# Performance work log

Hardware: AMD Instinct MI355X
Metric: run time of the kernel (lower is better)

## Reference

```python
import jax, jax.numpy as jnp
import numpy as np

N = 50000          # nodes
E = 800000         # edges (before self-loops)
IN_CH = 128
HID = 64
HEADS = 4
OUT_CH = 16
NEG_SLOPE = 0.2    # PyG GATConv default leaky_relu slope
EPS = 1e-16        # PyG softmax denominator epsilon


def glorot(key, shape):
    fan_in, fan_out = shape[0], shape[-1]
    lim = np.sqrt(6.0 / (fan_in + fan_out))
    return jax.random.uniform(key, shape, jnp.float32, -lim, lim)


def setup_inputs() -> dict:
    key = jax.random.key(0)
    ks = jax.random.split(key, 12)
    x = jax.random.normal(ks[0], (N, IN_CH), jnp.float32)
    edge_index = jax.random.randint(ks[1], (2, E), 0, N, jnp.int32)
    # layer 1: in -> HID per head, HEADS heads
    W1 = glorot(ks[2], (IN_CH, HEADS * HID))
    a_src1 = glorot(ks[3], (HEADS, HID))
    a_dst1 = glorot(ks[4], (HEADS, HID))
    b1 = jnp.zeros((HEADS * HID,), jnp.float32)
    # layer 2: HEADS*HID -> OUT_CH, 1 head
    W2 = glorot(ks[5], (HEADS * HID, OUT_CH))
    a_src2 = glorot(ks[6], (1, OUT_CH))
    a_dst2 = glorot(ks[7], (1, OUT_CH))
    b2 = jnp.zeros((OUT_CH,), jnp.float32)
    return {"x": x, "edge_index": edge_index,
            "W1": W1, "a_src1": a_src1, "a_dst1": a_dst1, "b1": b1,
            "W2": W2, "a_src2": a_src2, "a_dst2": a_dst2, "b2": b2}


def gat_conv(x, edge_index, W, a_src, a_dst, b, heads, ch):
    """PyG GATConv: linear, edge attention, segment softmax over dst, scatter-agg."""
    n = x.shape[0]
    loops = jnp.arange(n, dtype=edge_index.dtype)
    src = jnp.concatenate([edge_index[0], loops])   # add_self_loops=True
    dst = jnp.concatenate([edge_index[1], loops])
    h = (x @ W).reshape(n, heads, ch)               # [N, H, C]
    s_src = jnp.einsum('nhc,hc->nh', h, a_src)      # [N, H]
    s_dst = jnp.einsum('nhc,hc->nh', h, a_dst)
    e = s_src[src] + s_dst[dst]                     # [E', H]
    e = jnp.where(e > 0, e, NEG_SLOPE * e)          # leaky_relu
    m = jax.ops.segment_max(e, dst, num_segments=n)  # per-dst max
    ex = jnp.exp(e - m[dst])
    denom = jax.ops.segment_sum(ex, dst, num_segments=n)
    alpha = ex / (denom[dst] + EPS)                 # [E', H]
    out = jax.ops.segment_sum(h[src] * alpha[:, :, None], dst, num_segments=n)
    return out.reshape(n, heads * ch) + b


def reference(x, edge_index, W1, a_src1, a_dst1, b1, W2, a_src2, a_dst2, b2):
    h = gat_conv(x, edge_index, W1, a_src1, a_dst1, b1, HEADS, HID)
    h = jax.nn.elu(h)
    return gat_conv(h, edge_index, W2, a_src2, a_dst2, b2, 1, OUT_CH)
```

## Files before the change

### kernel.cpp

```cpp
#include <hip/hip_runtime.h>
#include <cstdint>
#include <cstddef>

#define NN 50000
#define IN_CH 128
#define C1 256
#define HID 64
#define HEADS 4
#define OUT_CH 16
#define NEG_SLOPE 0.2f
#define EPS_SM 1e-16f
#define NEGINF -3.4e38f
#define NBUK ((NN + 255) >> 8)

typedef __attribute__((ext_vector_type(8))) short bf16x8;
typedef __attribute__((ext_vector_type(4))) float f32x4;

__device__ __forceinline__ unsigned short f2b(float f) {
    unsigned int u = __float_as_uint(f);
    u += 0x7fffu + ((u >> 16) & 1u);
    return (unsigned short)(u >> 16);
}
__device__ __forceinline__ float b2f_lo(unsigned int packed) {
    return __uint_as_float(packed << 16);
}
__device__ __forceinline__ float b2f_hi(unsigned int packed) {
    return __uint_as_float(packed & 0xffff0000u);
}

__global__ void cvt_weights(const float* __restrict__ W1, const float* __restrict__ W2,
                            unsigned short* __restrict__ w1t, unsigned short* __restrict__ w2b) {
    int b = blockIdx.x, t = threadIdx.x;
    if (b < 128) {
        w1t[t * 128 + b] = f2b(W1[b * 256 + t]);
    } else {
        int k = (b - 128) * 16 + (t >> 4);
        int c = t & 15;
        w2b[c * 256 + k] = f2b(W2[k * 16 + c]);
    }
}

__global__ __launch_bounds__(256) void gemm1_mfma(const float* __restrict__ X,
                                                  const unsigned short* __restrict__ w1t,
                                                  const float* __restrict__ a_src1,
                                                  const float* __restrict__ a_dst1,
                                                  unsigned short* __restrict__ h1b,
                                                  float* __restrict__ ssrc1,
                                                  float* __restrict__ sdst1, int M) {
    __shared__ unsigned short xb[64 * 128];
    __shared__ unsigned short wt[256 * 128];
    int tid = threadIdx.x;
    int m0 = blockIdx.x * 64;
    {
        const uint4* gp = (const uint4*)w1t;
#pragma unroll
        for (int r = 0; r < 16; ++r) {
            int idx = r * 256 + tid;
            int byte = idx * 16;
            int row = byte >> 8;
            int cb = byte & 255;
            uint4 v = gp[idx];
            *(uint4*)((char*)wt + row * 256 + (cb ^ ((row & 7) << 4))) = v;
        }
    }
    {
#pragma unroll
        for (int r = 0; r < 8; ++r) {
            int f = r * 256 + tid;
            int e = f * 4;
            int row = e >> 7, col = e & 127;
            float4 v = make_float4(0.f, 0.f, 0.f, 0.f);
            if (m0 + row < M) v = *(const float4*)&X[(size_t)(m0 + row) * 128 + col];
            ushort4 bb;
            bb.x = f2b(v.x); bb.y = f2b(v.y); bb.z = f2b(v.z); bb.w = f2b(v.w);
            *(ushort4*)((char*)xb + row * 256 + ((col * 2) ^ ((row & 7) << 4))) = bb;
        }
    }
    __syncthreads();
    int wv = tid >> 6, l = tid & 63;
    int lm = l & 15, lk = l >> 4;
    int swz = (lm & 7) << 4;
    f32x4 acc[4][4];
#pragma unroll
    for (int a = 0; a < 4; ++a)
#pragma unroll
        for (int b = 0; b < 4; ++b) acc[a][b] = (f32x4){0.f, 0.f, 0.f, 0.f};
#pragma unroll
    for (int kk = 0; kk < 4; ++kk) {
        int kb = (kk * 64 + lk * 16) ^ swz;
        bf16x8 af[4], bfr[4];
#pragma unroll
        for (int mf = 0; mf < 4; ++mf)
            af[mf] = *(const bf16x8*)((const char*)xb + (mf * 16 + lm) * 256 + kb);
#pragma unroll
        for (int nt = 0; nt < 4; ++nt)
            bfr[nt] = *(const bf16x8*)((const char*)wt + (wv * 64 + nt * 16 + lm) * 256 + kb);
#pragma unroll
        for (int mf = 0; mf < 4; ++mf)
#pragma unroll
            for (int nt = 0; nt < 4; ++nt)
                acc[mf][nt] = __builtin_amdgcn_mfma_f32_16x16x32_bf16(af[mf], bfr[nt], acc[mf][nt], 0, 0, 0);
    }
#pragma unroll
    for (int mf = 0; mf < 4; ++mf) {
#pragma unroll
        for (int r = 0; r < 4; ++r) {
            int row = m0 + mf * 16 + lk * 4 + r;
            if (row < M) {
#pragma unroll
                for (int nt = 0; nt < 4; ++nt)
                    h1b[(size_t)row * 256 + wv * 64 + nt * 16 + lm] = f2b(acc[mf][nt][r]);
            }
        }
    }
    float av[4], dv[4];
#pragma unroll
    for (int nt = 0; nt < 4; ++nt) {
        av[nt] = a_src1[wv * 64 + nt * 16 + lm];
        dv[nt] = a_dst1[wv * 64 + nt * 16 + lm];
    }
#pragma unroll
    for (int mf = 0; mf < 4; ++mf) {
#pragma unroll
        for (int r = 0; r < 4; ++r) {
            float ps = acc[mf][0][r] * av[0] + acc[mf][1][r] * av[1]
                     + acc[mf][2][r] * av[2] + acc[mf][3][r] * av[3];
            float pd = acc[mf][0][r] * dv[0] + acc[mf][1][r] * dv[1]
                     + acc[mf][2][r] * dv[2] + acc[mf][3][r] * dv[3];
#pragma unroll
            for (int o = 1; o < 16; o <<= 1) {
                ps += __shfl_xor(ps, o);
                pd += __shfl_xor(pd, o);
            }
            if (lm == 0) {
                int row = m0 + mf * 16 + lk * 4 + r;
                if (row < M) {
                    ssrc1[row * HEADS + wv] = ps;
                    sdst1[row * HEADS + wv] = pd;
                }
            }
        }
    }
}

__global__ __launch_bounds__(256) void bucket_count(const int* __restrict__ dst_arr,
                                                    int* __restrict__ bcount,
                                                    int Etot, int E) {
    __shared__ int cnt[NBUK];
    int t = threadIdx.x;
    for (int i = t; i < NBUK; i += 256) cnt[i] = 0;
    __syncthreads();
    for (int i = blockIdx.x * 256 + t; i < Etot; i += gridDim.x * 256) {
        int dst = (i < E) ? dst_arr[i] : (i - E);
        atomicAdd(&cnt[dst >> 8], 1);
    }
    __syncthreads();
    for (int i = t; i < NBUK; i += 256)
        if (cnt[i]) atomicAdd(&bcount[i], cnt[i]);
}

__global__ __launch_bounds__(256) void bucket_scan(const int* __restrict__ bcount,
                                                   int* __restrict__ bbase,
                                                   int* __restrict__ bcursor,
                                                   int* __restrict__ rowst, int Etot) {
    __shared__ int s[256];
    int t = threadIdx.x;
    int x = (t < NBUK) ? bcount[t] : 0;
    s[t] = x;
    __syncthreads();
    for (int off = 1; off < 256; off <<= 1) {
        int v = (t >= off) ? s[t - off] : 0;
        __syncthreads();
        s[t] += v;
        __syncthreads();
    }
    int excl = s[t] - x;
    if (t < NBUK) {
        bbase[t] = excl;
        bcursor[t] = excl;
    }
    if (t == 0) {
        bbase[NBUK] = Etot;
        rowst[NN] = Etot;
    }
}

__global__ __launch_bounds__(256) void bucket_scatter(const int* __restrict__ src_arr,
                                                      const int* __restrict__ dst_arr,
                                                      int* __restrict__ bcursor,
                                                      unsigned int* __restrict__ ebuf,
                                                      int Etot, int E) {
    __shared__ int cnt[NBUK];
    __shared__ int cur[NBUK];
    int t = threadIdx.x;
    for (int i = t; i < NBUK; i += 256) cnt[i] = 0;
    __syncthreads();
    for (int i = blockIdx.x * 256 + t; i < Etot; i += gridDim.x * 256) {
        int dst = (i < E) ? dst_arr[i] : (i - E);
        atomicAdd(&cnt[dst >> 8], 1);
    }
    __syncthreads();
    for (int i = t; i < NBUK; i += 256)
        cur[i] = cnt[i] ? atomicAdd(&bcursor[i], cnt[i]) : 0;
    __syncthreads();
    for (int i = blockIdx.x * 256 + t; i < Etot; i += gridDim.x * 256) {
        int dst, src;
        if (i < E) { dst = dst_arr[i]; src = src_arr[i]; }
        else { dst = i - E; src = i - E; }
        int pos = atomicAdd(&cur[dst >> 8], 1);
        ebuf[pos] = ((unsigned int)(dst & 255) << 16) | (unsigned int)src;
    }
}

__global__ __launch_bounds__(256) void bucket_csr(const unsigned int* __restrict__ ebuf,
                                                  const int* __restrict__ bbase,
                                                  int* __restrict__ rowst,
                                                  int* __restrict__ srcs) {
    __shared__ int sdeg[256];
    __shared__ int scur[256];
    int t = threadIdx.x, b = blockIdx.x;
    int ebase = bbase[b], eend = bbase[b + 1];
    sdeg[t] = 0;
    __syncthreads();
    for (int i = ebase + t; i < eend; i += 256)
        atomicAdd(&sdeg[ebuf[i] >> 16], 1);
    __syncthreads();
    int x = sdeg[t];
    __syncthreads();
    for (int off = 1; off < 256; off <<= 1) {
        int v = (t >= off) ? sdeg[t - off] : 0;
        __syncthreads();
        sdeg[t] += v;
        __syncthreads();
    }
    int excl = sdeg[t] - x;
    int gnode = b * 256 + t;
    if (gnode < NN) rowst[gnode] = ebase + excl;
    scur[t] = excl;
    __syncthreads();
    for (int i = ebase + t; i < eend; i += 256) {
        unsigned int e = ebuf[i];
        int pos = atomicAdd(&scur[e >> 16], 1);
        srcs[ebase + pos] = (int)(e & 0xffffu);
    }
}

__global__ __launch_bounds__(256) void agg1_fused(const unsigned short* __restrict__ h1b,
                                                  const float* __restrict__ ssrc1,
                                                  const float* __restrict__ sdst1,
                                                  const int* __restrict__ row_start,
                                                  const int* __restrict__ srcs,
                                                  const float* __restrict__ b1,
                                                  unsigned short* __restrict__ out1b) {
    int d = blockIdx.x * 4 + (threadIdx.x >> 6);
    int l = threadIdx.x & 63;
    int start = row_start[d], end = row_start[d + 1];

    int sub = l & 15, h = l >> 4;
    float sdstA = sdst1[d * HEADS + h];
    auto comp = [&](int i) -> float {
        int s = srcs[i];
        float e = ssrc1[s * HEADS + h] + sdstA;
        return e > 0.f ? e : NEG_SLOPE * e;
    };
    float e0 = NEGINF, e1 = NEGINF, e2 = NEGINF, e3 = NEGINF;
    int i0 = start + sub;
    if (i0 < end) e0 = comp(i0);
    if (i0 + 16 < end) e1 = comp(i0 + 16);
    if (i0 + 32 < end) e2 = comp(i0 + 32);
    if (i0 + 48 < end) e3 = comp(i0 + 48);
    float mx = fmaxf(fmaxf(e0, e1), fmaxf(e2, e3));
    for (int i = i0 + 64; i < end; i += 16) mx = fmaxf(mx, comp(i));
#pragma unroll
    for (int o = 1; o < 16; o <<= 1) mx = fmaxf(mx, __shfl_xor(mx, o));
    float ssum = __expf(e0 - mx) + __expf(e1 - mx) + __expf(e2 - mx) + __expf(e3 - mx);
    for (int i = i0 + 64; i < end; i += 16) ssum += __expf(comp(i) - mx);
#pragma unroll
    for (int o = 1; o < 16; o <<= 1) ssum += __shfl_xor(ssum, o);
    float inv = 1.f / (ssum + EPS_SM);

    int half = l >> 5;
    int cl = l & 31;
    int hc = cl >> 3;
    float mxB = __shfl(mx, hc << 4);
    float invB = __shfl(inv, hc << 4);
    float sdstB = __shfl(sdstA, hc << 4);
    const int cb = cl * 8;
    auto alphaB = [&](int s) -> float {
        float e = ssrc1[s * HEADS + hc] + sdstB;
        e = e > 0.f ? e : NEG_SLOPE * e;
        return __expf(e - mxB) * invB;
    };
    float acc[8] = {};
    int i = start + half;
    for (; i + 6 < end; i += 8) {
        int s0 = srcs[i], s1 = srcs[i + 2], s2 = srcs[i + 4], s3 = srcs[i + 6];
        uint4 v0 = *(const uint4*)&h1b[(size_t)s0 * C1 + cb];
        uint4 v1 = *(const uint4*)&h1b[(size_t)s1 * C1 + cb];
        uint4 v2 = *(const uint4*)&h1b[(size_t)s2 * C1 + cb];
        uint4 v3 = *(const uint4*)&h1b[(size_t)s3 * C1 + cb];
        float a0 = alphaB(s0), a1 = alphaB(s1), a2 = alphaB(s2), a3 = alphaB(s3);
        acc[0] += a0 * b2f_lo(v0.x) + a1 * b2f_lo(v1.x) + a2 * b2f_lo(v2.x) + a3 * b2f_lo(v3.x);
        acc[1] += a0 * b2f_hi(v0.x) + a1 * b2f_hi(v1.x) + a2 * b2f_hi(v2.x) + a3 * b2f_hi(v3.x);
        acc[2] += a0 * b2f_lo(v0.y) + a1 * b2f_lo(v1.y) + a2 * b2f_lo(v2.y) + a3 * b2f_lo(v3.y);
        acc[3] += a0 * b2f_hi(v0.y) + a1 * b2f_hi(v1.y) + a2 * b2f_hi(v2.y) + a3 * b2f_hi(v3.y);
        acc[4] += a0 * b2f_lo(v0.z) + a1 * b2f_lo(v1.z) + a2 * b2f_lo(v2.z) + a3 * b2f_lo(v3.z);
        acc[5] += a0 * b2f_hi(v0.z) + a1 * b2f_hi(v1.z) + a2 * b2f_hi(v2.z) + a3 * b2f_hi(v3.z);
        acc[6] += a0 * b2f_lo(v0.w) + a1 * b2f_lo(v1.w) + a2 * b2f_lo(v2.w) + a3 * b2f_lo(v3.w);
        acc[7] += a0 * b2f_hi(v0.w) + a1 * b2f_hi(v1.w) + a2 * b2f_hi(v2.w) + a3 * b2f_hi(v3.w);
    }
    for (; i < end; i += 2) {
        int s = srcs[i];
        uint4 v = *(const uint4*)&h1b[(size_t)s * C1 + cb];
        float a = alphaB(s);
        acc[0] += a * b2f_lo(v.x); acc[1] += a * b2f_hi(v.x);
        acc[2] += a * b2f_lo(v.y); acc[3] += a * b2f_hi(v.y);
        acc[4] += a * b2f_lo(v.z); acc[5] += a * b2f_hi(v.z);
        acc[6] += a * b2f_lo(v.w); acc[7] += a * b2f_hi(v.w);
    }
#pragma unroll
    for (int j = 0; j < 8; ++j) acc[j] += __shfl_xor(acc[j], 32);
    if (half == 0) {
        float4 ba = *(const float4*)&b1[cb];
        float4 bbv = *(const float4*)&b1[cb + 4];
        float v[8];
        v[0] = acc[0] + ba.x;  v[1] = acc[1] + ba.y;
        v[2] = acc[2] + ba.z;  v[3] = acc[3] + ba.w;
        v[4] = acc[4] + bbv.x; v[5] = acc[5] + bbv.y;
        v[6] = acc[6] + bbv.z; v[7] = acc[7] + bbv.w;
        bf16x8 o;
#pragma unroll
        for (int j = 0; j < 8; ++j) {
            float t = v[j] > 0.f ? v[j] : (__expf(v[j]) - 1.f);
            o[j] = (short)f2b(t);
        }
        *(bf16x8*)&out1b[(size_t)d * C1 + cb] = o;
    }
}

__global__ __launch_bounds__(256) void gemm2_mfma(const unsigned short* __restrict__ out1b,
                                                  const unsigned short* __restrict__ w2b,
                                                  const float* __restrict__ a_src2,
                                                  const float* __restrict__ a_dst2,
                                                  float* __restrict__ h2,
                                                  float* __restrict__ ssrc2,
                                                  float* __restrict__ sdst2, int M) {
    __shared__ char ab[64 * 528];
    int tid = threadIdx.x;
    int m0 = blockIdx.x * 64;
#pragma unroll
    for (int r = 0; r < 8; ++r) {
        int byte = r * 4096 + tid * 16;
        int row = byte >> 9, col = byte & 511;
        uint4 v = make_uint4(0u, 0u, 0u, 0u);
        if (m0 + row < M)
            v = *(const uint4*)((const char*)out1b + (size_t)(m0 + row) * 512 + col);
        *(uint4*)(ab + row * 528 + col) = v;
    }
    int wv = tid >> 6, l = tid & 63;
    int lm = l & 15, lk = l >> 4;
    bf16x8 bfr[8];
#pragma unroll
    for (int kk = 0; kk < 8; ++kk)
        bfr[kk] = *(const bf16x8*)&w2b[lm * 256 + lk * 8 + kk * 32];
    __syncthreads();
    f32x4 acc = (f32x4){0.f, 0.f, 0.f, 0.f};
    const char* base = ab + (wv * 16 + lm) * 528 + lk * 16;
#pragma unroll
    for (int kk = 0; kk < 8; ++kk) {
        bf16x8 af = *(const bf16x8*)(base + kk * 64);
        acc = __builtin_amdgcn_mfma_f32_16x16x32_bf16(af, bfr[kk], acc, 0, 0, 0);
    }
    float asc = a_src2[lm], adc = a_dst2[lm];
#pragma unroll
    for (int r = 0; r < 4; ++r) {
        int grow = m0 + wv * 16 + lk * 4 + r;
        float v = acc[r];
        float ps = v * asc, pd = v * adc;
#pragma unroll
        for (int o = 1; o < 16; o <<= 1) {
            ps += __shfl_xor(ps, o);
            pd += __shfl_xor(pd, o);
        }
        if (grow < M) {
            h2[(size_t)grow * OUT_CH + lm] = v;
            if (lm == 0) {
                ssrc2[grow] = ps;
                sdst2[grow] = pd;
            }
        }
    }
}

__global__ __launch_bounds__(256) void agg2_fused(const float* __restrict__ h2,
                                                  const float* __restrict__ ssrc2,
                                                  const float* __restrict__ sdst2,
                                                  const int* __restrict__ row_start,
                                                  const int* __restrict__ srcs,
                                                  const float* __restrict__ b2,
                                                  float* __restrict__ out) {
    int d = blockIdx.x * 4 + (threadIdx.x >> 6);
    int l = threadIdx.x & 63;
    int start = row_start[d], end = row_start[d + 1];
    float sdst = sdst2[d];
    auto comp = [&](int i) -> float {
        int s = srcs[i];
        float e = ssrc2[s] + sdst;
        return e > 0.f ? e : NEG_SLOPE * e;
    };
    float e0 = NEGINF, e1 = NEGINF;
    int i0 = start + l;
    if (i0 < end) e0 = comp(i0);
    if (i0 + 64 < end) e1 = comp(i0 + 64);
    float mx = fmaxf(e0, e1);
    for (int i = i0 + 128; i < end; i += 64) mx = fmaxf(mx, comp(i));
#pragma unroll
    for (int o = 1; o < 64; o <<= 1) mx = fmaxf(mx, __shfl_xor(mx, o));
    float ssum = __expf(e0 - mx) + __expf(e1 - mx);
    for (int i = i0 + 128; i < end; i += 64) ssum += __expf(comp(i) - mx);
#pragma unroll
    for (int o = 1; o < 64; o <<= 1) ssum += __shfl_xor(ssum, o);
    float inv = 1.f / (ssum + EPS_SM);

    int slot = l >> 2;
    int c4 = (l & 3) * 4;
    float4 acc = make_float4(0.f, 0.f, 0.f, 0.f);
    for (int i = start + slot; i < end; i += 16) {
        int s = srcs[i];
        float e = ssrc2[s] + sdst;
        e = e > 0.f ? e : NEG_SLOPE * e;
        float a = __expf(e - mx) * inv;
        float4 v = *(const float4*)&h2[(size_t)s * OUT_CH + c4];
        acc.x += a * v.x; acc.y += a * v.y; acc.z += a * v.z; acc.w += a * v.w;
    }
#pragma unroll
    for (int o = 4; o < 64; o <<= 1) {
        acc.x += __shfl_xor(acc.x, o);
        acc.y += __shfl_xor(acc.y, o);
        acc.z += __shfl_xor(acc.z, o);
        acc.w += __shfl_xor(acc.w, o);
    }
    if (l < 4) {
        float4 bb = *(const float4*)&b2[c4];
        float4 r = make_float4(acc.x + bb.x, acc.y + bb.y, acc.z + bb.z, acc.w + bb.w);
        *(float4*)&out[(size_t)d * OUT_CH + c4] = r;
    }
}

extern "C" void kernel_launch(void* const* d_in, const int* in_sizes, int n_in,
                              void* d_out, int out_size, void* d_ws, size_t ws_size,
                              hipStream_t stream) {
    const float* x      = (const float*)d_in[0];
    const int*   ei     = (const int*)d_in[1];
    const float* W1     = (const float*)d_in[2];
    const float* a_src1 = (const float*)d_in[3];
    const float* a_dst1 = (const float*)d_in[4];
    const float* b1     = (const float*)d_in[5];
    const float* W2     = (const float*)d_in[6];
    const float* a_src2 = (const float*)d_in[7];
    const float* a_dst2 = (const float*)d_in[8];
    const float* b2     = (const float*)d_in[9];
    float* out = (float*)d_out;

    const int E = in_sizes[1] / 2;
    const int Etot = E + NN;
    const int* src_arr = ei;
    const int* dst_arr = ei + E;

    size_t off = 0;
    auto carve = [&](size_t bytes) -> void* {
        void* r = (char*)d_ws + off;
        off += (bytes + 255) & ~(size_t)255;
        return r;
    };
    unsigned short* h1b  = (unsigned short*)carve((size_t)NN * C1 * 2);
    unsigned short* out1b= (unsigned short*)carve((size_t)NN * C1 * 2);
    unsigned short* w1t  = (unsigned short*)carve((size_t)IN_CH * C1 * 2);
    unsigned short* w2b  = (unsigned short*)carve((size_t)C1 * OUT_CH * 2);
    float* ssrc1 = (float*)carve((size_t)NN * HEADS * 4);
    float* sdst1 = (float*)carve((size_t)NN * HEADS * 4);
    float* h2    = (float*)carve((size_t)NN * OUT_CH * 4);
    float* ssrc2 = (float*)carve((size_t)NN * 4);
    float* sdst2 = (float*)carve((size_t)NN * 4);
    int* rowst   = (int*)carve((size_t)(NN + 1) * 4);
    int* srcs    = (int*)carve((size_t)Etot * 4);
    unsigned int* ebuf = (unsigned int*)carve((size_t)Etot * 4);
    int* bcount  = (int*)carve((size_t)NBUK * 4);
    int* bbase   = (int*)carve((size_t)(NBUK + 1) * 4);
    int* bcursor = (int*)carve((size_t)NBUK * 4);

    hipMemsetAsync(bcount, 0, (size_t)NBUK * 4, stream);
    bucket_count<<<256, 256, 0, stream>>>(dst_arr, bcount, Etot, E);
    bucket_scan<<<1, 256, 0, stream>>>(bcount, bbase, bcursor, rowst, Etot);
    bucket_scatter<<<256, 256, 0, stream>>>(src_arr, dst_arr, bcursor, ebuf, Etot, E);
    bucket_csr<<<NBUK, 256, 0, stream>>>(ebuf, bbase, rowst, srcs);

    cvt_weights<<<144, 256, 0, stream>>>(W1, W2, w1t, w2b);

    gemm1_mfma<<<(NN + 63) / 64, 256, 0, stream>>>(x, w1t, a_src1, a_dst1,
                                                   h1b, ssrc1, sdst1, NN);
    agg1_fused<<<NN / 4, 256, 0, stream>>>(h1b, ssrc1, sdst1, rowst, srcs, b1, out1b);

    gemm2_mfma<<<(NN + 63) / 64, 256, 0, stream>>>(out1b, w2b, a_src2, a_dst2,
                                                   h2, ssrc2, sdst2, NN);
    agg2_fused<<<NN / 4, 256, 0, stream>>>(h2, ssrc2, sdst2, rowst, srcs, b2, out);
}
```

Before: 173.1 us.

## Fold attention vectors into W1 via extra MFMA and cache softmax weights in LDS

Attention score projections for layer 1 are precomputed as W1·a_src/a_dst in bf16 and computed with one extra MFMA per row fragment, replacing the per-wave shuffle reductions in the GEMM epilogue. Both aggregation kernels now store the normalized softmax weights from the first pass in shared memory and reuse them in the gather loop for nodes with small degree. This avoids re-gathering source scores and recomputing exp per edge. In exchange, the scores are computed from bf16-rounded folded weights, which lowers their precision, and a fallback path handles high-degree nodes.

```diff
diff --git a/kernel.cpp b/kernel.cpp
--- a/kernel.cpp
+++ b/kernel.cpp
@@ -29,21 +29,40 @@
 }
 
 __global__ void cvt_weights(const float* __restrict__ W1, const float* __restrict__ W2,
-                            unsigned short* __restrict__ w1t, unsigned short* __restrict__ w2b) {
+                            const float* __restrict__ a_src1, const float* __restrict__ a_dst1,
+                            unsigned short* __restrict__ w1t, unsigned short* __restrict__ w2b,
+                            unsigned short* __restrict__ waSDt) {
     int b = blockIdx.x, t = threadIdx.x;
     if (b < 128) {
         w1t[t * 128 + b] = f2b(W1[b * 256 + t]);
-    } else {
+    } else if (b < 144) {
         int k = (b - 128) * 16 + (t >> 4);
         int c = t & 15;
         w2b[c * 256 + k] = f2b(W2[k * 16 + c]);
+    } else {
+        if (t < 128) {
+            const float* wrow = W1 + t * 256;
+#pragma unroll
+            for (int h = 0; h < 4; ++h) {
+                float ss = 0.f, sd = 0.f;
+#pragma unroll
+                for (int c = 0; c < 64; ++c) {
+                    float w = wrow[h * 64 + c];
+                    ss += w * a_src1[h * 64 + c];
+                    sd += w * a_dst1[h * 64 + c];
+                }
+                waSDt[h * 128 + t] = f2b(ss);
+                waSDt[(4 + h) * 128 + t] = f2b(sd);
+            }
+#pragma unroll
+            for (int c = 8; c < 16; ++c) waSDt[c * 128 + t] = 0;
+        }
     }
 }
 
 __global__ __launch_bounds__(256) void gemm1_mfma(const float* __restrict__ X,
                                                   const unsigned short* __restrict__ w1t,
-                                                  const float* __restrict__ a_src1,
-                                                  const float* __restrict__ a_dst1,
+                                                  const unsigned short* __restrict__ waSDt,
                                                   unsigned short* __restrict__ h1b,
                                                   float* __restrict__ ssrc1,
                                                   float* __restrict__ sdst1, int M) {
@@ -80,11 +99,18 @@
     int wv = tid >> 6, l = tid & 63;
     int lm = l & 15, lk = l >> 4;
     int swz = (lm & 7) << 4;
+    bf16x8 sfr[4];
+#pragma unroll
+    for (int kk = 0; kk < 4; ++kk)
+        sfr[kk] = *(const bf16x8*)&waSDt[lm * 128 + kk * 32 + lk * 8];
     f32x4 acc[4][4];
-#pragma unroll
-    for (int a = 0; a < 4; ++a)
+    f32x4 accS[4];
+#pragma unroll
+    for (int a = 0; a < 4; ++a) {
+        accS[a] = (f32x4){0.f, 0.f, 0.f, 0.f};
 #pragma unroll
         for (int b = 0; b < 4; ++b) acc[a][b] = (f32x4){0.f, 0.f, 0.f, 0.f};
+    }
 #pragma unroll
     for (int kk = 0; kk < 4; ++kk) {
         int kb = (kk * 64 + lk * 16) ^ swz;
@@ -96,10 +122,12 @@
         for (int nt = 0; nt < 4; ++nt)
             bfr[nt] = *(const bf16x8*)((const char*)wt + (wv * 64 + nt * 16 + lm) * 256 + kb);
 #pragma unroll
-        for (int mf = 0; mf < 4; ++mf)
+        for (int mf = 0; mf < 4; ++mf) {
 #pragma unroll
             for (int nt = 0; nt < 4; ++nt)
                 acc[mf][nt] = __builtin_amdgcn_mfma_f32_16x16x32_bf16(af[mf], bfr[nt], acc[mf][nt], 0, 0, 0);
+            accS[mf] = __builtin_amdgcn_mfma_f32_16x16x32_bf16(af[mf], sfr[kk], accS[mf], 0, 0, 0);
+        }
     }
 #pragma unroll
     for (int mf = 0; mf < 4; ++mf) {
@@ -113,31 +141,14 @@
             }
         }
     }
-    float av[4], dv[4];
-#pragma unroll
-    for (int nt = 0; nt < 4; ++nt) {
-        av[nt] = a_src1[wv * 64 + nt * 16 + lm];
-        dv[nt] = a_dst1[wv * 64 + nt * 16 + lm];
-    }
-#pragma unroll
-    for (int mf = 0; mf < 4; ++mf) {
+    {
+        f32x4 as = accS[wv];
 #pragma unroll
         for (int r = 0; r < 4; ++r) {
-            float ps = acc[mf][0][r] * av[0] + acc[mf][1][r] * av[1]
-                     + acc[mf][2][r] * av[2] + acc[mf][3][r] * av[3];
-            float pd = acc[mf][0][r] * dv[0] + acc[mf][1][r] * dv[1]
-                     + acc[mf][2][r] * dv[2] + acc[mf][3][r] * dv[3];
-#pragma unroll
-            for (int o = 1; o < 16; o <<= 1) {
-                ps += __shfl_xor(ps, o);
-                pd += __shfl_xor(pd, o);
-            }
-            if (lm == 0) {
-                int row = m0 + mf * 16 + lk * 4 + r;
-                if (row < M) {
-                    ssrc1[row * HEADS + wv] = ps;
-                    sdst1[row * HEADS + wv] = pd;
-                }
+            int row = m0 + wv * 16 + lk * 4 + r;
+            if (row < M && lm < 8) {
+                if (lm < 4) ssrc1[row * HEADS + lm] = as[r];
+                else        sdst1[row * HEADS + (lm - 4)] = as[r];
             }
         }
     }
@@ -252,9 +263,12 @@
                                                   const int* __restrict__ srcs,
                                                   const float* __restrict__ b1,
                                                   unsigned short* __restrict__ out1b) {
-    int d = blockIdx.x * 4 + (threadIdx.x >> 6);
+    __shared__ float alds[4][64][4];
+    int wid = threadIdx.x >> 6;
+    int d = blockIdx.x * 4 + wid;
     int l = threadIdx.x & 63;
     int start = row_start[d], end = row_start[d + 1];
+    int deg = end - start;
 
     int sub = l & 15, h = l >> 4;
     float sdstA = sdst1[d * HEADS + h];
@@ -273,50 +287,68 @@
     for (int i = i0 + 64; i < end; i += 16) mx = fmaxf(mx, comp(i));
 #pragma unroll
     for (int o = 1; o < 16; o <<= 1) mx = fmaxf(mx, __shfl_xor(mx, o));
-    float ssum = __expf(e0 - mx) + __expf(e1 - mx) + __expf(e2 - mx) + __expf(e3 - mx);
+    float s0 = __expf(e0 - mx), s1 = __expf(e1 - mx);
+    float s2 = __expf(e2 - mx), s3 = __expf(e3 - mx);
+    float ssum = s0 + s1 + s2 + s3;
     for (int i = i0 + 64; i < end; i += 16) ssum += __expf(comp(i) - mx);
 #pragma unroll
     for (int o = 1; o < 16; o <<= 1) ssum += __shfl_xor(ssum, o);
     float inv = 1.f / (ssum + EPS_SM);
+    alds[wid][sub][h] = s0 * inv;
+    alds[wid][sub + 16][h] = s1 * inv;
+    alds[wid][sub + 32][h] = s2 * inv;
+    alds[wid][sub + 48][h] = s3 * inv;
 
     int half = l >> 5;
     int cl = l & 31;
     int hc = cl >> 3;
-    float mxB = __shfl(mx, hc << 4);
-    float invB = __shfl(inv, hc << 4);
-    float sdstB = __shfl(sdstA, hc << 4);
     const int cb = cl * 8;
-    auto alphaB = [&](int s) -> float {
-        float e = ssrc1[s * HEADS + hc] + sdstB;
-        e = e > 0.f ? e : NEG_SLOPE * e;
-        return __expf(e - mxB) * invB;
-    };
     float acc[8] = {};
     int i = start + half;
-    for (; i + 6 < end; i += 8) {
-        int s0 = srcs[i], s1 = srcs[i + 2], s2 = srcs[i + 4], s3 = srcs[i + 6];
-        uint4 v0 = *(const uint4*)&h1b[(size_t)s0 * C1 + cb];
-        uint4 v1 = *(const uint4*)&h1b[(size_t)s1 * C1 + cb];
-        uint4 v2 = *(const uint4*)&h1b[(size_t)s2 * C1 + cb];
-        uint4 v3 = *(const uint4*)&h1b[(size_t)s3 * C1 + cb];
-        float a0 = alphaB(s0), a1 = alphaB(s1), a2 = alphaB(s2), a3 = alphaB(s3);
-        acc[0] += a0 * b2f_lo(v0.x) + a1 * b2f_lo(v1.x) + a2 * b2f_lo(v2.x) + a3 * b2f_lo(v3.x);
-        acc[1] += a0 * b2f_hi(v0.x) + a1 * b2f_hi(v1.x) + a2 * b2f_hi(v2.x) + a3 * b2f_hi(v3.x);
-        acc[2] += a0 * b2f_lo(v0.y) + a1 * b2f_lo(v1.y) + a2 * b2f_lo(v2.y) + a3 * b2f_lo(v3.y);
-        acc[3] += a0 * b2f_hi(v0.y) + a1 * b2f_hi(v1.y) + a2 * b2f_hi(v2.y) + a3 * b2f_hi(v3.y);
-        acc[4] += a0 * b2f_lo(v0.z) + a1 * b2f_lo(v1.z) + a2 * b2f_lo(v2.z) + a3 * b2f_lo(v3.z);
-        acc[5] += a0 * b2f_hi(v0.z) + a1 * b2f_hi(v1.z) + a2 * b2f_hi(v2.z) + a3 * b2f_hi(v3.z);
-        acc[6] += a0 * b2f_lo(v0.w) + a1 * b2f_lo(v1.w) + a2 * b2f_lo(v2.w) + a3 * b2f_lo(v3.w);
-        acc[7] += a0 * b2f_hi(v0.w) + a1 * b2f_hi(v1.w) + a2 * b2f_hi(v2.w) + a3 * b2f_hi(v3.w);
-    }
-    for (; i < end; i += 2) {
-        int s = srcs[i];
-        uint4 v = *(const uint4*)&h1b[(size_t)s * C1 + cb];
-        float a = alphaB(s);
-        acc[0] += a * b2f_lo(v.x); acc[1] += a * b2f_hi(v.x);
-        acc[2] += a * b2f_lo(v.y); acc[3] += a * b2f_hi(v.y);
-        acc[4] += a * b2f_lo(v.z); acc[5] += a * b2f_hi(v.z);
-        acc[6] += a * b2f_lo(v.w); acc[7] += a * b2f_hi(v.w);
+    if (deg <= 64) {
+        for (; i + 6 < end; i += 8) {
+            int s0_ = srcs[i], s1_ = srcs[i + 2], s2_ = srcs[i + 4], s3_ = srcs[i + 6];
+            uint4 v0 = *(const uint4*)&h1b[(size_t)s0_ * C1 + cb];
+            uint4 v1 = *(const uint4*)&h1b[(size_t)s1_ * C1 + cb];
+            uint4 v2 = *(const uint4*)&h1b[(size_t)s2_ * C1 + cb];
+            uint4 v3 = *(const uint4*)&h1b[(size_t)s3_ * C1 + cb];
+            float a0 = alds[wid][i - start][hc];
+            float a1 = alds[wid][i + 2 - start][hc];
+            float a2 = alds[wid][i + 4 - start][hc];
+            float a3 = alds[wid][i + 6 - start][hc];
+            acc[0] += a0 * b2f_lo(v0.x) + a1 * b2f_lo(v1.x) + a2 * b2f_lo(v2.x) + a3 * b2f_lo(v3.x);
+            acc[1] += a0 * b2f_hi(v0.x) + a1 * b2f_hi(v1.x) + a2 * b2f_hi(v2.x) + a3 * b2f_hi(v3.x);
+            acc[2] += a0 * b2f_lo(v0.y) + a1 * b2f_lo(v1.y) + a2 * b2f_lo(v2.y) + a3 * b2f_lo(v3.y);
+            acc[3] += a0 * b2f_hi(v0.y) + a1 * b2f_hi(v1.y) + a2 * b2f_hi(v2.y) + a3 * b2f_hi(v3.y);
+            acc[4] += a0 * b2f_lo(v0.z) + a1 * b2f_lo(v1.z) + a2 * b2f_lo(v2.z) + a3 * b2f_lo(v3.z);
+            acc[5] += a0 * b2f_hi(v0.z) + a1 * b2f_hi(v1.z) + a2 * b2f_hi(v2.z) + a3 * b2f_hi(v3.z);
+            acc[6] += a0 * b2f_lo(v0.w) + a1 * b2f_lo(v1.w) + a2 * b2f_lo(v2.w) + a3 * b2f_lo(v3.w);
+            acc[7] += a0 * b2f_hi(v0.w) + a1 * b2f_hi(v1.w) + a2 * b2f_hi(v2.w) + a3 * b2f_hi(v3.w);
+        }
+        for (; i < end; i += 2) {
+            int s = srcs[i];
+            uint4 v = *(const uint4*)&h1b[(size_t)s * C1 + cb];
+            float a = alds[wid][i - start][hc];
+            acc[0] += a * b2f_lo(v.x); acc[1] += a * b2f_hi(v.x);
+            acc[2] += a * b2f_lo(v.y); acc[3] += a * b2f_hi(v.y);
+            acc[4] += a * b2f_lo(v.z); acc[5] += a * b2f_hi(v.z);
+            acc[6] += a * b2f_lo(v.w); acc[7] += a * b2f_hi(v.w);
+        }
+    } else {
+        float mxB = __shfl(mx, hc << 4);
+        float invB = __shfl(inv, hc << 4);
+        float sdstB = __shfl(sdstA, hc << 4);
+        for (; i < end; i += 2) {
+            int s = srcs[i];
+            uint4 v = *(const uint4*)&h1b[(size_t)s * C1 + cb];
+            float e = ssrc1[s * HEADS + hc] + sdstB;
+            e = e > 0.f ? e : NEG_SLOPE * e;
+            float a = __expf(e - mxB) * invB;
+            acc[0] += a * b2f_lo(v.x); acc[1] += a * b2f_hi(v.x);
+            acc[2] += a * b2f_lo(v.y); acc[3] += a * b2f_hi(v.y);
+            acc[4] += a * b2f_lo(v.z); acc[5] += a * b2f_hi(v.z);
+            acc[6] += a * b2f_lo(v.w); acc[7] += a * b2f_hi(v.w);
+        }
     }
 #pragma unroll
     for (int j = 0; j < 8; ++j) acc[j] += __shfl_xor(acc[j], 32);
@@ -399,9 +431,12 @@
                                                   const int* __restrict__ srcs,
                                                   const float* __restrict__ b2,
                                                   float* __restrict__ out) {
-    int d = blockIdx.x * 4 + (threadIdx.x >> 6);
+    __shared__ float alds[4][128];
+    int wid = threadIdx.x >> 6;
+    int d = blockIdx.x * 4 + wid;
     int l = threadIdx.x & 63;
     int start = row_start[d], end = row_start[d + 1];
+    int deg = end - start;
     float sdst = sdst2[d];
     auto comp = [&](int i) -> float {
         int s = srcs[i];
@@ -416,22 +451,34 @@
     for (int i = i0 + 128; i < end; i += 64) mx = fmaxf(mx, comp(i));
 #pragma unroll
     for (int o = 1; o < 64; o <<= 1) mx = fmaxf(mx, __shfl_xor(mx, o));
-    float ssum = __expf(e0 - mx) + __expf(e1 - mx);
+    float s0 = __expf(e0 - mx), s1 = __expf(e1 - mx);
+    float ssum = s0 + s1;
     for (int i = i0 + 128; i < end; i += 64) ssum += __expf(comp(i) - mx);
 #pragma unroll
     for (int o = 1; o < 64; o <<= 1) ssum += __shfl_xor(ssum, o);
     float inv = 1.f / (ssum + EPS_SM);
+    alds[wid][l] = s0 * inv;
+    alds[wid][l + 64] = s1 * inv;
 
     int slot = l >> 2;
     int c4 = (l & 3) * 4;
     float4 acc = make_float4(0.f, 0.f, 0.f, 0.f);
-    for (int i = start + slot; i < end; i += 16) {
-        int s = srcs[i];
-        float e = ssrc2[s] + sdst;
-        e = e > 0.f ? e : NEG_SLOPE * e;
-        float a = __expf(e - mx) * inv;
-        float4 v = *(const float4*)&h2[(size_t)s * OUT_CH + c4];
-        acc.x += a * v.x; acc.y += a * v.y; acc.z += a * v.z; acc.w += a * v.w;
+    if (deg <= 128) {
+        for (int i = start + slot; i < end; i += 16) {
+            int s = srcs[i];
+            float a = alds[wid][i - start];
+            float4 v = *(const float4*)&h2[(size_t)s * OUT_CH + c4];
+            acc.x += a * v.x; acc.y += a * v.y; acc.z += a * v.z; acc.w += a * v.w;
+        }
+    } else {
+        for (int i = start + slot; i < end; i += 16) {
+            int s = srcs[i];
+            float e = ssrc2[s] + sdst;
+            e = e > 0.f ? e : NEG_SLOPE * e;
+            float a = __expf(e - mx) * inv;
+            float4 v = *(const float4*)&h2[(size_t)s * OUT_CH + c4];
+            acc.x += a * v.x; acc.y += a * v.y; acc.z += a * v.z; acc.w += a * v.w;
+        }
     }
 #pragma unroll
     for (int o = 4; o < 64; o <<= 1) {
@@ -477,6 +524,7 @@
     unsigned short* out1b= (unsigned short*)carve((size_t)NN * C1 * 2);
     unsigned short* w1t  = (unsigned short*)carve((size_t)IN_CH * C1 * 2);
     unsigned short* w2b  = (unsigned short*)carve((size_t)C1 * OUT_CH * 2);
+    unsigned short* waSDt= (unsigned short*)carve((size_t)16 * 128 * 2);
     float* ssrc1 = (float*)carve((size_t)NN * HEADS * 4);
     float* sdst1 = (float*)carve((size_t)NN * HEADS * 4);
     float* h2    = (float*)carve((size_t)NN * OUT_CH * 4);
@@ -495,10 +543,9 @@
     bucket_scatter<<<256, 256, 0, stream>>>(src_arr, dst_arr, bcursor, ebuf, Etot, E);
     bucket_csr<<<NBUK, 256, 0, stream>>>(ebuf, bbase, rowst, srcs);
 
-    cvt_weights<<<144, 256, 0, stream>>>(W1, W2, w1t, w2b);
-
-    gemm1_mfma<<<(NN + 63) / 64, 256, 0, stream>>>(x, w1t, a_src1, a_dst1,
-                                                   h1b, ssrc1, sdst1, NN);
+    cvt_weights<<<145, 256, 0, stream>>>(W1, W2, a_src1, a_dst1, w1t, w2b, waSDt);
+
+    gemm1_mfma<<<(NN + 63) / 64, 256, 0, stream>>>(x, w1t, waSDt, h1b, ssrc1, sdst1, NN);
     agg1_fused<<<NN / 4, 256, 0, stream>>>(h1b, ssrc1, sdst1, rowst, srcs, b1, out1b);
 
     gemm2_mfma<<<(NN + 63) / 64, 256, 0, stream>>>(out1b, w2b, a_src2, a_dst2,
```

Result: no change. 171.6 us (-0.9%).
